# Kernel tuning notes

Hardware: AMD Instinct MI355X
Metric: run time of the kernel (lower is better)

Reference implementation:

```python
import jax, jax.numpy as jnp
import numpy as np

B, N, H, L, E, OUT = 32, 128, 128, 3, 65536, 128
AV, BV = 128, 16  # atom / bond feature vocab sizes
NEG = -1e9


def setup_inputs() -> dict:
    key = jax.random.key(0)
    ks = jax.random.split(key, 20)
    x = jax.random.randint(ks[0], (B * N, 9), 0, AV)          # OGB atom features
    edge_attr = jax.random.randint(ks[1], (E, 3), 0, BV)      # OGB bond features
    # within-graph random edges (PyG requires edges not to cross graphs)
    g = jax.random.randint(ks[2], (E,), 0, B)
    src = jax.random.randint(ks[3], (E,), 0, N)
    dst = jax.random.randint(ks[4], (E,), 0, N)
    edge_index = jnp.stack([g * N + src, g * N + dst])        # [2, E] global node ids
    batch_idx = jnp.repeat(jnp.arange(B), N)                  # equal-size graphs
    s = 0.05
    w = lambda k, *shape: jax.random.normal(k, shape, dtype=jnp.float32) * s
    return {
        "x": x, "edge_attr": edge_attr, "edge_index": edge_index, "batch_idx": batch_idx,
        "atom_emb": w(ks[5], 9, AV, H), "bond_emb": w(ks[6], 3, BV, H),
        "Wm1": w(ks[7], L, 2 * H, H), "bm1": jnp.zeros((L, H), jnp.float32),
        "Wm2": w(ks[8], L, 2 * H, H), "bm2": jnp.zeros((L, H), jnp.float32),
        "We": w(ks[9], L, H, H), "be": jnp.zeros((L, H), jnp.float32),
        "Wg": w(ks[10], L, H, H), "bg": jnp.zeros((L, H), jnp.float32),
        "Wp1": w(ks[11], L, H, H), "bp1": jnp.zeros((L, H), jnp.float32),
        "Wp2": w(ks[12], L, H, H), "bp2": jnp.zeros((L, H), jnp.float32),
        "Wo1": w(ks[13], L, 2 * H, H), "bo1": jnp.zeros((L, H), jnp.float32),
        "Wo2": w(ks[14], L, H, H), "bo2": jnp.zeros((L, H), jnp.float32),
        "ln_s": jnp.ones((L, H), jnp.float32), "ln_b": jnp.zeros((L, H), jnp.float32),
        "Wh1": w(ks[15], H, H), "bh1": jnp.zeros((H,), jnp.float32),
        "Wh2": w(ks[16], H, OUT), "bh2": jnp.zeros((OUT,), jnp.float32),
    }


def reference(x, edge_attr, edge_index, batch_idx, atom_emb, bond_emb,
              Wm1, bm1, Wm2, bm2, We, be, Wg, bg, Wp1, bp1, Wp2, bp2,
              Wo1, bo1, Wo2, bo2, ln_s, ln_b, Wh1, bh1, Wh2, bh2):
    # AtomEncoder / BondEncoder: sum of per-column embeddings
    node_fts = jnp.sum(atom_emb[jnp.arange(9), x], axis=1)        # [B*N, H]
    edge_fts = jnp.sum(bond_emb[jnp.arange(3), edge_attr], axis=1)  # [E, H]
    # to_dense_batch with equal-size graphs == reshape; mask all-True
    node_fts = node_fts.reshape(B, N, H)
    # to_dense_adj: scatter-add edge list into dense [B, N, N] (+features)
    g = edge_index[0] // N
    s_loc = edge_index[0] % N
    d_loc = edge_index[1] % N
    adj = jnp.zeros((B, N, N), jnp.float32).at[g, s_loc, d_loc].add(1.0)
    edge_dense = jnp.zeros((B, N, N, H), jnp.float32).at[g, s_loc, d_loc].add(edge_fts)
    graph_fts = jnp.zeros((B, H), jnp.float32)
    hidden = jnp.zeros_like(node_fts)
    adj_mask = (adj > 0)[..., None]                               # [B, Ns, Nr, 1]
    for l in range(L):  # CLRS-style MPNN layers
        z = jnp.concatenate([node_fts, hidden], axis=-1)          # [B, N, 2H]
        m1 = z @ Wm1[l] + bm1[l]
        m2 = z @ Wm2[l] + bm2[l]
        me = edge_dense @ We[l] + be[l]
        mg = graph_fts @ Wg[l] + bg[l]
        msgs = m1[:, :, None, :] + m2[:, None, :, :] + me + mg[:, None, None, :]
        msgs = jax.nn.relu(msgs)
        msgs = jax.nn.relu(msgs @ Wp1[l] + bp1[l]) @ Wp2[l] + bp2[l]  # msgs MLP [H,H]
        msgs = jnp.max(jnp.where(adj_mask, msgs, NEG), axis=1)   # masked max over senders
        h = jax.nn.relu(z @ Wo1[l] + bo1[l] + msgs @ Wo2[l] + bo2[l])
        mu = h.mean(-1, keepdims=True)
        var = ((h - mu) ** 2).mean(-1, keepdims=True)
        hidden = (h - mu) / jnp.sqrt(var + 1e-5) * ln_s[l] + ln_b[l]
    # masked mean pool (mask is all-True here) + prediction MLP
    graph_emb = hidden.mean(axis=1)                               # [B, H]
    return jax.nn.relu(graph_emb @ Wh1 + bh1) @ Wh2 + bh2         # [B, OUT]
```

## Files before the change

kernel.cpp:

```cpp
#include <hip/hip_runtime.h>
#include <hip/hip_bf16.h>

#define NB_ 32
#define LL_ 3
#define EE_ 65536
#define NODES_ 4096
#define SLOTS_ 524288
#define NEGV -1e9f

typedef _Float16 f16x8 __attribute__((ext_vector_type(8)));
typedef float f32x4 __attribute__((ext_vector_type(4)));

__device__ __forceinline__ unsigned fkey(float f) {
  unsigned b = __float_as_uint(f);
  unsigned m = ((int)b >> 31) | 0x80000000u;
  return b ^ m;
}
__device__ __forceinline__ float funkey(unsigned k) {
  unsigned xm = (k & 0x80000000u) ? 0x80000000u : 0xFFFFFFFFu;
  return __uint_as_float(k ^ xm);
}

__global__ __launch_bounds__(256) void k_pro(const int* __restrict__ x,
    const float* __restrict__ atom_emb, _Float16* __restrict__ zh,
    const float* __restrict__ Wp1, const float* __restrict__ Wp2,
    const float* __restrict__ Wm1, const float* __restrict__ Wm2,
    const float* __restrict__ Wo1, const float* __restrict__ Wo2,
    _Float16* __restrict__ Whf,
    const float* __restrict__ bond_emb, const float* __restrict__ We,
    _Float16* __restrict__ bembWeh,
    const int* __restrict__ ei, int* __restrict__ cnt, int* __restrict__ erank) {
  int blk = blockIdx.x, tid = threadIdx.x;
  if (blk < 2048) {
    int v = blk * 2 + (tid >> 7), t = tid & 127;
    float acc = 0.f;
#pragma unroll
    for (int c = 0; c < 9; c++) {
      int xv = x[v * 9 + c];
      acc += atom_emb[(c * 128 + xv) * 128 + t];
    }
    zh[v * 256 + t] = (_Float16)acc;
    zh[v * 256 + 128 + t] = (_Float16)0.f;
  } else if (blk < 2264) {
    int gid = (blk - 2048) * 256 + tid;
    int lane = gid & 63;
    int llo = lane & 15, lhi = lane >> 4;
    const float* W; int col, kbase;
    if (gid < 12288) {
      int mat = gid >> 11, pos = gid & 2047;
      int fr = pos >> 6; int ct = fr >> 2, kt = fr & 3;
      int lyr = mat >> 1, which = mat & 1;
      W = (which ? Wp2 : Wp1) + lyr * 16384;
      col = ct * 16 + llo; kbase = kt * 32 + lhi * 8;
    } else if (gid < 36864) {
      int q = gid - 12288;
      int lyr = q >> 13, r = q & 8191;
      int fr = r >> 6; int ct = fr >> 3, kt = fr & 7;
      col = ct * 16 + llo; kbase = kt * 32 + lhi * 8;
      if (col < 128) { W = Wm1 + lyr * 32768; }
      else { W = Wm2 + lyr * 32768; col -= 128; }
    } else {
      int q = gid - 36864;
      int lyr = q / 6144, r = q % 6144;
      int fr = r >> 6; int ct = fr / 12, kt = fr % 12;
      col = ct * 16 + llo; kbase = kt * 32 + lhi * 8;
      if (kbase < 256) { W = Wo1 + lyr * 32768; }
      else { W = Wo2 + lyr * 16384; kbase -= 256; }
    }
    f16x8 h;
#pragma unroll
    for (int e = 0; e < 8; e++) h[e] = (_Float16)W[(kbase + e) * 128 + col];
    ((f16x8*)Whf)[gid] = h;
  } else if (blk < 2336) {
    __shared__ float row[2][128];
    int rid = (blk - 2264) * 2 + (tid >> 7);
    int half = tid >> 7, c = tid & 127;
    int l = rid / 48, rr = rid % 48;
    row[half][c] = bond_emb[rr * 128 + c];
    __syncthreads();
    const float* W = We + l * 16384;
    float acc = 0.f;
    for (int k = 0; k < 128; k += 4) {
      acc += row[half][k] * W[k * 128 + c] +
             row[half][k + 1] * W[(k + 1) * 128 + c] +
             row[half][k + 2] * W[(k + 2) * 128 + c] +
             row[half][k + 3] * W[(k + 3) * 128 + c];
    }
    bembWeh[(l * 48 + rr) * 128 + c] = (_Float16)acc;
  } else {
    int e = (blk - 2336) * 256 + tid;
    int s = ei[e], d = ei[EE_ + e];
    int g = s >> 7, i = s & 127, j = d & 127;
    int slot = ((g << 7) + j) * 128 + i;
    erank[e] = atomicAdd(&cnt[slot], 1);
  }
}

__global__ __launch_bounds__(256) void k_scanA(const int* __restrict__ cnt,
    int* __restrict__ basep, int* __restrict__ pairbase,
    int* __restrict__ bsumA, int* __restrict__ bsumF) {
  __shared__ int sA[256], sF[256];
  int t = threadIdx.x, gid = blockIdx.x * 256 + t;
  int v = cnt[gid];
  int f = v > 0 ? 1 : 0;
  sA[t] = v; sF[t] = f; __syncthreads();
  for (int st = 1; st < 256; st <<= 1) {
    int aA = sA[t], aF = sF[t];
    int bA = (t >= st) ? sA[t - st] : 0;
    int bF = (t >= st) ? sF[t - st] : 0;
    __syncthreads();
    sA[t] = aA + bA; sF[t] = aF + bF;
    __syncthreads();
  }
  basep[gid] = sA[t] - v;
  pairbase[gid] = sF[t] - f;
  if (t == 255) { bsumA[blockIdx.x] = sA[255]; bsumF[blockIdx.x] = sF[255]; }
}

__global__ __launch_bounds__(256) void k_scan2d(int* __restrict__ bsumA,
                                                int* __restrict__ bsumF) {
  int* bsum = blockIdx.x ? bsumF : bsumA;
  __shared__ int s[256];
  int t = threadIdx.x;
  int v[8]; int tot = 0;
#pragma unroll
  for (int q = 0; q < 8; q++) { v[q] = bsum[t * 8 + q]; tot += v[q]; }
  s[t] = tot; __syncthreads();
  for (int st = 1; st < 256; st <<= 1) {
    int a = s[t]; int b = (t >= st) ? s[t - st] : 0;
    __syncthreads(); s[t] = a + b; __syncthreads();
  }
  int run = s[t] - tot;
#pragma unroll
  for (int q = 0; q < 8; q++) { int tmp = v[q]; bsum[t * 8 + q] = run; run += tmp; }
}

__global__ __launch_bounds__(256) void k_scanBS(const int* __restrict__ cnt,
    const int* __restrict__ basep, const int* __restrict__ pairbase,
    const int* __restrict__ bsumA, const int* __restrict__ bsumF,
    int* __restrict__ pair_total, int* __restrict__ pair_slot,
    int* __restrict__ pair_off, int* __restrict__ pair_cnt,
    const int* __restrict__ ei, const int* __restrict__ erank,
    int* __restrict__ sorted_e) {
  int blk = blockIdx.x, tid = threadIdx.x;
  if (blk < 2048) {
    int gid = blk * 256 + tid;
    int b = basep[gid] + bsumA[gid >> 8];
    int pb = pairbase[gid] + bsumF[gid >> 8];
    int c = cnt[gid];
    if (c > 0) {
      pair_slot[pb] = gid;
      pair_off[pb] = b;
      pair_cnt[pb] = c;
    }
    if (gid == SLOTS_ - 1) pair_total[0] = pb + (c > 0 ? 1 : 0);
  } else {
    int e = (blk - 2048) * 256 + tid;
    int s = ei[e], d = ei[EE_ + e];
    int g = s >> 7, i = s & 127, j = d & 127;
    int slot = ((g << 7) + j) * 128 + i;
    int pos = basep[slot] + bsumA[slot >> 8] + erank[e];
    sorted_e[pos] = e;
  }
}

__global__ __launch_bounds__(256, 4) void k_m12(const _Float16* __restrict__ zh,
    const _Float16* __restrict__ Whf, const float* __restrict__ bm1,
    const float* __restrict__ bm2, _Float16* __restrict__ mm,
    unsigned* __restrict__ msgs_u, int l) {
  int tid = threadIdx.x;
  {
    int g0 = blockIdx.x * 256 + tid;
    unsigned kneg = fkey(NEGV);
    msgs_u[g0] = kneg;
    msgs_u[g0 + 262144] = kneg;
  }
  int wv = tid >> 6, l64 = tid & 63;
  int llo = l64 & 15, lhi = l64 >> 4;
  int tile = blockIdx.x >> 2;
  int ct = (blockIdx.x & 3) * 4 + wv;
  int row = tile * 16 + llo;
  f16x8 a[8];
#pragma unroll
  for (int kt = 0; kt < 8; kt++)
    a[kt] = *(const f16x8*)(zh + row * 256 + kt * 32 + lhi * 8);
  const f16x8* Bf = (const f16x8*)Whf + 12288 + l * 8192;
  int col = ct * 16 + llo;
  float bv = (col < 128) ? bm1[l * 128 + col] : bm2[l * 128 + col - 128];
  f32x4 acc = {bv, bv, bv, bv};
#pragma unroll
  for (int kt = 0; kt < 8; kt++)
    acc = __builtin_amdgcn_mfma_f32_16x16x32_f16(a[kt], Bf[(ct * 8 + kt) * 64 + l64], acc, 0, 0, 0);
#pragma unroll
  for (int reg = 0; reg < 4; reg++)
    mm[(tile * 16 + lhi * 4 + reg) * 256 + col] = (_Float16)acc[reg];
}

__global__ __launch_bounds__(256, 4) void k_pairs(
    const _Float16* __restrict__ mm,
    const int* __restrict__ pair_slot, const int* __restrict__ pair_off,
    const int* __restrict__ pair_cnt, const int* __restrict__ pair_total,
    const int* __restrict__ sorted_e, const int* __restrict__ edge_attr,
    const _Float16* __restrict__ bembWeh,
    const float* __restrict__ be, const float* __restrict__ bg,
    const _Float16* __restrict__ Whf,
    const float* __restrict__ bp1, const float* __restrict__ bp2,
    unsigned* __restrict__ msgs_u, int l) {
  __shared__ int s_slot[64], s_off[64], s_cnt[64], s_lrow[64];
  __shared__ int s_scan[64];
  __shared__ int s_rid[16];
  __shared__ int s_nrecv;
  __shared__ unsigned Lmax[16 * 128];
  __shared__ _Float16 Uh[64 * 128];
  int P = pair_total[0];
  int pid0 = blockIdx.x * 64;
  if (pid0 >= P) return;
  int tid = threadIdx.x;
  {
    unsigned kneg = fkey(NEGV);
#pragma unroll
    for (int q = 0; q < 8; q++) Lmax[tid + q * 256] = kneg;
  }
  if (tid < 64) {
    int pid = pid0 + tid;
    bool va = pid < P;
    s_slot[tid] = va ? pair_slot[pid] : -1;
    s_off[tid] = va ? pair_off[pid] : 0;
    s_cnt[tid] = va ? pair_cnt[pid] : 0;
  }
  __syncthreads();
  if (tid < 64) {
    int slot = s_slot[tid];
    int r = slot >= 0 ? (slot >> 7) : -1;
    int pr = (tid == 0) ? -2 : (s_slot[tid - 1] >= 0 ? (s_slot[tid - 1] >> 7) : -1);
    s_scan[tid] = (slot >= 0 && r != pr) ? 1 : 0;
  }
  __syncthreads();
  for (int st = 1; st < 64; st <<= 1) {
    int a = 0, b = 0;
    if (tid < 64) { a = s_scan[tid]; b = (tid >= st) ? s_scan[tid - st] : 0; }
    __syncthreads();
    if (tid < 64) s_scan[tid] = a + b;
    __syncthreads();
  }
  if (tid < 64) {
    int slot = s_slot[tid];
    int lr = s_scan[tid] - 1;
    s_lrow[tid] = lr;
    int r = slot >= 0 ? (slot >> 7) : -1;
    int pr = (tid == 0) ? -2 : (s_slot[tid - 1] >= 0 ? (s_slot[tid - 1] >> 7) : -1);
    if (slot >= 0 && r != pr && lr < 16) s_rid[lr] = r;
    if (tid == 63) s_nrecv = s_scan[63];
  }
  __syncthreads();

  int l64 = tid & 63, wv = tid >> 6;
  int llo = l64 & 15, lhi = l64 >> 4;
  int p = wv * 16 + llo;
  int slot = s_slot[p];
  f16x8 a[4];
  if (slot >= 0) {
    int rr = slot >> 7, i = slot & 127, g = slot >> 14;
    int sn = (g << 7) + i;
    float t32[4][8];
#pragma unroll
    for (int kt = 0; kt < 4; kt++) {
      int c0 = kt * 32 + lhi * 8;
      f16x8 v1 = *(const f16x8*)(mm + sn * 256 + c0);
      f16x8 v2 = *(const f16x8*)(mm + rr * 256 + 128 + c0);
      float4 e0 = *(const float4*)(be + l * 128 + c0);
      float4 e1 = *(const float4*)(be + l * 128 + c0 + 4);
      float4 g0 = *(const float4*)(bg + l * 128 + c0);
      float4 g1 = *(const float4*)(bg + l * 128 + c0 + 4);
      t32[kt][0] = (float)v1[0] + (float)v2[0] + e0.x + g0.x;
      t32[kt][1] = (float)v1[1] + (float)v2[1] + e0.y + g0.y;
      t32[kt][2] = (float)v1[2] + (float)v2[2] + e0.z + g0.z;
      t32[kt][3] = (float)v1[3] + (float)v2[3] + e0.w + g0.w;
      t32[kt][4] = (float)v1[4] + (float)v2[4] + e1.x + g1.x;
      t32[kt][5] = (float)v1[5] + (float)v2[5] + e1.y + g1.y;
      t32[kt][6] = (float)v1[6] + (float)v2[6] + e1.z + g1.z;
      t32[kt][7] = (float)v1[7] + (float)v2[7] + e1.w + g1.w;
    }
    int off = s_off[p], cn = s_cnt[p];
    for (int d = 0; d < cn; d++) {
      int eid = sorted_e[off + d];
      int a0 = edge_attr[eid * 3], a1 = edge_attr[eid * 3 + 1],
          a2 = edge_attr[eid * 3 + 2];
      const _Float16* r0 = bembWeh + (l * 48 + a0) * 128;
      const _Float16* r1 = bembWeh + (l * 48 + 16 + a1) * 128;
      const _Float16* r2 = bembWeh + (l * 48 + 32 + a2) * 128;
#pragma unroll
      for (int kt = 0; kt < 4; kt++) {
        int c0 = kt * 32 + lhi * 8;
        f16x8 x0 = *(const f16x8*)(r0 + c0);
        f16x8 x1 = *(const f16x8*)(r1 + c0);
        f16x8 x2 = *(const f16x8*)(r2 + c0);
#pragma unroll
        for (int e = 0; e < 8; e++)
          t32[kt][e] += (float)x0[e] + (float)x1[e] + (float)x2[e];
      }
    }
#pragma unroll
    for (int kt = 0; kt < 4; kt++)
#pragma unroll
      for (int e = 0; e < 8; e++) a[kt][e] = (_Float16)fmaxf(t32[kt][e], 0.f);
  } else {
#pragma unroll
    for (int kt = 0; kt < 4; kt++)
#pragma unroll
      for (int e = 0; e < 8; e++) a[kt][e] = (_Float16)0.f;
  }

  const f16x8* W1f = (const f16x8*)Whf + (l * 2) * 2048;
  const f16x8* W2f = (const f16x8*)Whf + (l * 2 + 1) * 2048;
#pragma unroll
  for (int ct = 0; ct < 8; ct++) {
    int col = ct * 16 + llo;
    float b1 = bp1[l * 128 + col];
    f32x4 acc = {b1, b1, b1, b1};
#pragma unroll
    for (int kt = 0; kt < 4; kt++)
      acc = __builtin_amdgcn_mfma_f32_16x16x32_f16(a[kt], W1f[(ct * 4 + kt) * 64 + l64], acc, 0, 0, 0);
#pragma unroll
    for (int reg = 0; reg < 4; reg++) {
      int wrow = wv * 16 + lhi * 4 + reg;
      int sg = (2 * ct + (llo >> 3)) ^ (wrow & 15);
      Uh[wrow * 128 + sg * 8 + (llo & 7)] = (_Float16)fmaxf(acc[reg], 0.f);
    }
  }
  __syncthreads();
  f16x8 a2[4];
  int arow = wv * 16 + llo;
#pragma unroll
  for (int kt = 0; kt < 4; kt++) {
    int sg = (kt * 4 + lhi) ^ (arow & 15);
    a2[kt] = *(const f16x8*)(Uh + arow * 128 + sg * 8);
  }
#pragma unroll
  for (int ct = 0; ct < 8; ct++) {
    int col = ct * 16 + llo;
    float b2 = bp2[l * 128 + col];
    f32x4 acc = {b2, b2, b2, b2};
#pragma unroll
    for (int kt = 0; kt < 4; kt++)
      acc = __builtin_amdgcn_mfma_f32_16x16x32_f16(a2[kt], W2f[(ct * 4 + kt) * 64 + l64], acc, 0, 0, 0);
    int prev_lr = -2, prev_rr = -1; float run = 0.f;
#pragma unroll
    for (int reg = 0; reg < 4; reg++) {
      int prow = wv * 16 + lhi * 4 + reg;
      int slot2 = s_slot[prow];
      if (slot2 < 0) continue;
      int lr = s_lrow[prow];
      float v = acc[reg];
      if (lr == prev_lr) {
        run = fmaxf(run, v);
      } else {
        if (prev_lr >= 0) {
          if (prev_lr < 16) atomicMax(&Lmax[prev_lr * 128 + col], fkey(run));
          else atomicMax(&msgs_u[prev_rr * 128 + col], fkey(run));
        }
        prev_lr = lr; prev_rr = slot2 >> 7; run = v;
      }
    }
    if (prev_lr >= 0) {
      if (prev_lr < 16) atomicMax(&Lmax[prev_lr * 128 + col], fkey(run));
      else atomicMax(&msgs_u[prev_rr * 128 + col], fkey(run));
    }
  }
  __syncthreads();
  int nr = s_nrecv; if (nr > 16) nr = 16;
  for (int base = 0; base < nr; base += 2) {
    int lr = base + (tid >> 7);
    int col = tid & 127;
    if (lr < nr)
      atomicMax(&msgs_u[s_rid[lr] * 128 + col], Lmax[lr * 128 + col]);
  }
}

__global__ __launch_bounds__(512, 2) void k_olnm12(_Float16* __restrict__ zh,
    unsigned* __restrict__ msgs_u, const _Float16* __restrict__ Whf,
    const float* __restrict__ bo1, const float* __restrict__ bo2,
    const float* __restrict__ ln_s, const float* __restrict__ ln_b,
    const float* __restrict__ bm1, const float* __restrict__ bm2,
    _Float16* __restrict__ mm, int l) {
  __shared__ float sumA[8][16];
  __shared__ float muS[16], rsS[16];
  __shared__ _Float16 hidT[16][132];
  int tid = threadIdx.x;
  int wv = tid >> 6, l64 = tid & 63;
  int llo = l64 & 15, lhi = l64 >> 4;
  int row = blockIdx.x * 16 + llo;
  f16x8 a[12];
#pragma unroll
  for (int kt = 0; kt < 8; kt++)
    a[kt] = *(const f16x8*)(zh + row * 256 + kt * 32 + lhi * 8);
#pragma unroll
  for (int kt = 8; kt < 12; kt++) {
    int k0 = (kt - 8) * 32 + lhi * 8;
    f16x8 h;
#pragma unroll
    for (int e = 0; e < 8; e++) {
      float v = funkey(msgs_u[row * 128 + k0 + e]);
      v = fmaxf(fminf(v, 60000.f), -60000.f);
      h[e] = (_Float16)v;
    }
    a[kt] = h;
  }
  const f16x8* Bo = (const f16x8*)Whf + 36864 + l * 6144;
  int ct = wv, col = ct * 16 + llo;
  float bv = bo1[l * 128 + col] + bo2[l * 128 + col];
  f32x4 acc = {bv, bv, bv, bv};
#pragma unroll
  for (int kt = 0; kt < 12; kt++)
    acc = __builtin_amdgcn_mfma_f32_16x16x32_f16(a[kt], Bo[(ct * 12 + kt) * 64 + l64], acc, 0, 0, 0);
  float h[4];
#pragma unroll
  for (int reg = 0; reg < 4; reg++) h[reg] = fmaxf(acc[reg], 0.f);
#pragma unroll
  for (int reg = 0; reg < 4; reg++) {
    float s = h[reg];
    s += __shfl_xor(s, 1, 64); s += __shfl_xor(s, 2, 64);
    s += __shfl_xor(s, 4, 64); s += __shfl_xor(s, 8, 64);
    if (llo == 0) sumA[wv][lhi * 4 + reg] = s;
  }
  __syncthreads();
  if (tid < 16) {
    float s = 0.f;
#pragma unroll
    for (int w = 0; w < 8; w++) s += sumA[w][tid];
    muS[tid] = s * (1.f / 128.f);
  }
  __syncthreads();
#pragma unroll
  for (int reg = 0; reg < 4; reg++) {
    float d = h[reg] - muS[lhi * 4 + reg];
    float s = d * d;
    s += __shfl_xor(s, 1, 64); s += __shfl_xor(s, 2, 64);
    s += __shfl_xor(s, 4, 64); s += __shfl_xor(s, 8, 64);
    if (llo == 0) sumA[wv][lhi * 4 + reg] = s;
  }
  __syncthreads();
  if (tid < 16) {
    float s = 0.f;
#pragma unroll
    for (int w = 0; w < 8; w++) s += sumA[w][tid];
    rsS[tid] = rsqrtf(s * (1.f / 128.f) + 1e-5f);
  }
  __syncthreads();
  float sc = ln_s[l * 128 + col], bb = ln_b[l * 128 + col];
#pragma unroll
  for (int reg = 0; reg < 4; reg++) {
    int rr = lhi * 4 + reg;
    int wrow = blockIdx.x * 16 + rr;
    _Float16 hh = (_Float16)((h[reg] - muS[rr]) * rsS[rr] * sc + bb);
    zh[wrow * 256 + 128 + col] = hh;
    hidT[rr][col] = hh;
  }
  {
    unsigned kneg = fkey(NEGV);
    int base = blockIdx.x * 2048 + tid;
    msgs_u[base] = kneg;
    msgs_u[base + 512] = kneg;
    msgs_u[base + 1024] = kneg;
    msgs_u[base + 1536] = kneg;
  }
  __syncthreads();
  f16x8 b[4];
#pragma unroll
  for (int kt = 0; kt < 4; kt++)
    b[kt] = *(const f16x8*)(&hidT[llo][kt * 32 + lhi * 8]);
  const f16x8* Bm = (const f16x8*)Whf + 12288 + (l + 1) * 8192;
#pragma unroll
  for (int q = 0; q < 2; q++) {
    int ct2 = wv + q * 8;
    int col2 = ct2 * 16 + llo;
    float bv2 = (col2 < 128) ? bm1[(l + 1) * 128 + col2]
                             : bm2[(l + 1) * 128 + col2 - 128];
    f32x4 acc2 = {bv2, bv2, bv2, bv2};
#pragma unroll
    for (int kt = 0; kt < 4; kt++)
      acc2 = __builtin_amdgcn_mfma_f32_16x16x32_f16(a[kt], Bm[(ct2 * 8 + kt) * 64 + l64], acc2, 0, 0, 0);
#pragma unroll
    for (int kt = 0; kt < 4; kt++)
      acc2 = __builtin_amdgcn_mfma_f32_16x16x32_f16(b[kt], Bm[(ct2 * 8 + 4 + kt) * 64 + l64], acc2, 0, 0, 0);
#pragma unroll
    for (int reg = 0; reg < 4; reg++)
      mm[(blockIdx.x * 16 + lhi * 4 + reg) * 256 + col2] = (_Float16)acc2[reg];
  }
}

__global__ __launch_bounds__(512, 2) void k_out_ln(_Float16* __restrict__ zh,
    const unsigned* __restrict__ msgs_u, const _Float16* __restrict__ Whf,
    const float* __restrict__ bo1, const float* __restrict__ bo2,
    const float* __restrict__ ln_s, const float* __restrict__ ln_b, int l) {
  __shared__ float sumA[8][16];
  __shared__ float muS[16], rsS[16];
  int tid = threadIdx.x;
  int wv = tid >> 6, l64 = tid & 63;
  int llo = l64 & 15, lhi = l64 >> 4;
  int row = blockIdx.x * 16 + llo;
  f16x8 a[12];
#pragma unroll
  for (int kt = 0; kt < 8; kt++)
    a[kt] = *(const f16x8*)(zh + row * 256 + kt * 32 + lhi * 8);
#pragma unroll
  for (int kt = 8; kt < 12; kt++) {
    int k0 = (kt - 8) * 32 + lhi * 8;
    f16x8 h;
#pragma unroll
    for (int e = 0; e < 8; e++) {
      float v = funkey(msgs_u[row * 128 + k0 + e]);
      v = fmaxf(fminf(v, 60000.f), -60000.f);
      h[e] = (_Float16)v;
    }
    a[kt] = h;
  }
  const f16x8* Bf = (const f16x8*)Whf + 36864 + l * 6144;
  int ct = wv, col = ct * 16 + llo;
  float bv = bo1[l * 128 + col] + bo2[l * 128 + col];
  f32x4 acc = {bv, bv, bv, bv};
#pragma unroll
  for (int kt = 0; kt < 12; kt++)
    acc = __builtin_amdgcn_mfma_f32_16x16x32_f16(a[kt], Bf[(ct * 12 + kt) * 64 + l64], acc, 0, 0, 0);
  float h[4];
#pragma unroll
  for (int reg = 0; reg < 4; reg++) h[reg] = fmaxf(acc[reg], 0.f);
#pragma unroll
  for (int reg = 0; reg < 4; reg++) {
    float s = h[reg];
    s += __shfl_xor(s, 1, 64); s += __shfl_xor(s, 2, 64);
    s += __shfl_xor(s, 4, 64); s += __shfl_xor(s, 8, 64);
    if (llo == 0) sumA[wv][lhi * 4 + reg] = s;
  }
  __syncthreads();
  if (tid < 16) {
    float s = 0.f;
#pragma unroll
    for (int w = 0; w < 8; w++) s += sumA[w][tid];
    muS[tid] = s * (1.f / 128.f);
  }
  __syncthreads();
#pragma unroll
  for (int reg = 0; reg < 4; reg++) {
    float d = h[reg] - muS[lhi * 4 + reg];
    float s = d * d;
    s += __shfl_xor(s, 1, 64); s += __shfl_xor(s, 2, 64);
    s += __shfl_xor(s, 4, 64); s += __shfl_xor(s, 8, 64);
    if (llo == 0) sumA[wv][lhi * 4 + reg] = s;
  }
  __syncthreads();
  if (tid < 16) {
    float s = 0.f;
#pragma unroll
    for (int w = 0; w < 8; w++) s += sumA[w][tid];
    rsS[tid] = rsqrtf(s * (1.f / 128.f) + 1e-5f);
  }
  __syncthreads();
  float sc = ln_s[l * 128 + col], bb = ln_b[l * 128 + col];
#pragma unroll
  for (int reg = 0; reg < 4; reg++) {
    int rr = lhi * 4 + reg;
    int wrow = blockIdx.x * 16 + rr;
    zh[wrow * 256 + 128 + col] =
        (_Float16)((h[reg] - muS[rr]) * rsS[rr] * sc + bb);
  }
}

__global__ __launch_bounds__(128) void k_head(const _Float16* __restrict__ zh,
    const float* __restrict__ Wh1, const float* __restrict__ bh1,
    const float* __restrict__ Wh2, const float* __restrict__ bh2,
    float* __restrict__ out) {
  __shared__ float ge[128], p1[128];
  int b = blockIdx.x, t = threadIdx.x;
  float s = 0.f;
  for (int n = 0; n < 128; n++) s += (float)zh[(b * 128 + n) * 256 + 128 + t];
  ge[t] = s * (1.f / 128.f);
  __syncthreads();
  float a = bh1[t];
  for (int k = 0; k < 128; k++) a += ge[k] * Wh1[k * 128 + t];
  p1[t] = fmaxf(a, 0.f);
  __syncthreads();
  float o = bh2[t];
  for (int k = 0; k < 128; k++) o += p1[k] * Wh2[k * 128 + t];
  out[b * 128 + t] = o;
}

extern "C" void kernel_launch(void* const* d_in, const int* in_sizes, int n_in,
                              void* d_out, int out_size, void* d_ws, size_t ws_size,
                              hipStream_t stream) {
  const int* x          = (const int*)d_in[0];
  const int* edge_attr  = (const int*)d_in[1];
  const int* edge_index = (const int*)d_in[2];
  const float* atom_emb = (const float*)d_in[4];
  const float* bond_emb = (const float*)d_in[5];
  const float* Wm1 = (const float*)d_in[6];
  const float* bm1 = (const float*)d_in[7];
  const float* Wm2 = (const float*)d_in[8];
  const float* bm2 = (const float*)d_in[9];
  const float* We  = (const float*)d_in[10];
  const float* be  = (const float*)d_in[11];
  const float* bg  = (const float*)d_in[13];
  const float* Wp1 = (const float*)d_in[14];
  const float* bp1 = (const float*)d_in[15];
  const float* Wp2 = (const float*)d_in[16];
  const float* bp2 = (const float*)d_in[17];
  const float* Wo1 = (const float*)d_in[18];
  const float* bo1 = (const float*)d_in[19];
  const float* Wo2 = (const float*)d_in[20];
  const float* bo2 = (const float*)d_in[21];
  const float* ln_s = (const float*)d_in[22];
  const float* ln_b = (const float*)d_in[23];
  const float* Wh1 = (const float*)d_in[24];
  const float* bh1 = (const float*)d_in[25];
  const float* Wh2 = (const float*)d_in[26];
  const float* bh2 = (const float*)d_in[27];
  float* out = (float*)d_out;

  int* cnt       = (int*)d_ws;
  int* basep     = cnt + SLOTS_;
  int* pairbase  = basep + SLOTS_;
  int* bsumA     = pairbase + SLOTS_;
  int* bsumF     = bsumA + 2048;
  int* pair_tot  = bsumF + 2048;
  int* erank     = pair_tot + 16;
  int* sorted_e  = erank + EE_;
  int* pair_slot = sorted_e + EE_;
  int* pair_off  = pair_slot + EE_;
  int* pair_cnt  = pair_off + EE_;
  unsigned* msgs_u = (unsigned*)(pair_cnt + EE_);
  _Float16* zh   = (_Float16*)(msgs_u + SLOTS_);
  _Float16* mm   = zh + NODES_ * 256;
  _Float16* bembWeh = mm + NODES_ * 256;
  _Float16* Whf  = bembWeh + 3 * 48 * 128;

  hipMemsetAsync(cnt, 0, SLOTS_ * sizeof(int), stream);

  k_pro<<<2592, 256, 0, stream>>>(x, atom_emb, zh, Wp1, Wp2, Wm1, Wm2, Wo1, Wo2,
                                  Whf, bond_emb, We, bembWeh, edge_index, cnt,
                                  erank);
  k_scanA<<<SLOTS_ / 256, 256, 0, stream>>>(cnt, basep, pairbase, bsumA, bsumF);
  k_scan2d<<<2, 256, 0, stream>>>(bsumA, bsumF);
  k_scanBS<<<2304, 256, 0, stream>>>(cnt, basep, pairbase, bsumA, bsumF,
                                     pair_tot, pair_slot, pair_off, pair_cnt,
                                     edge_index, erank, sorted_e);

  k_m12<<<1024, 256, 0, stream>>>(zh, Whf, bm1, bm2, mm, msgs_u, 0);
  k_pairs<<<1024, 256, 0, stream>>>(mm, pair_slot, pair_off, pair_cnt,
                                    pair_tot, sorted_e, edge_attr, bembWeh,
                                    be, bg, Whf, bp1, bp2, msgs_u, 0);
  k_olnm12<<<NODES_ / 16, 512, 0, stream>>>(zh, msgs_u, Whf, bo1, bo2, ln_s,
                                            ln_b, bm1, bm2, mm, 0);
  k_pairs<<<1024, 256, 0, stream>>>(mm, pair_slot, pair_off, pair_cnt,
                                    pair_tot, sorted_e, edge_attr, bembWeh,
                                    be, bg, Whf, bp1, bp2, msgs_u, 1);
  k_olnm12<<<NODES_ / 16, 512, 0, stream>>>(zh, msgs_u, Whf, bo1, bo2, ln_s,
                                            ln_b, bm1, bm2, mm, 1);
  k_pairs<<<1024, 256, 0, stream>>>(mm, pair_slot, pair_off, pair_cnt,
                                    pair_tot, sorted_e, edge_attr, bembWeh,
                                    be, bg, Whf, bp1, bp2, msgs_u, 2);
  k_out_ln<<<NODES_ / 16, 512, 0, stream>>>(zh, msgs_u, Whf, bo1, bo2,
                                            ln_s, ln_b, 2);
  k_head<<<NB_, 128, 0, stream>>>(zh, Wh1, bh1, Wh2, bh2, out);
}
```

Before: 257.3 us.

## Fuse scan stages with last-block election and merge first m12 GEMM into scatter

Removes the separate second-level scan kernel: the last block of the first scan (found through an atomic counter) scans the per-block sums itself. The first layer's m1/m2 GEMM and msgs init are merged into the scatter kernel as extra blocks. The pair-grouping prefix scan in k_pairs now uses wavefront shuffles instead of shared-memory steps with barriers. This cuts two kernel launches and several barriers, at the cost of atomics, fences, and a serial tail in the elected block.

Result: slower. 310.3 us (+20.6%).

```diff
diff --git a/kernel.cpp b/kernel.cpp
--- a/kernel.cpp
+++ b/kernel.cpp
@@ -96,11 +96,12 @@
   }
 }
 
-__global__ __launch_bounds__(256) void k_scanA(const int* __restrict__ cnt,
+__global__ __launch_bounds__(256) void k_scanA2(const int* __restrict__ cnt,
     int* __restrict__ basep, int* __restrict__ pairbase,
-    int* __restrict__ bsumA, int* __restrict__ bsumF) {
+    int* __restrict__ bsumA, int* __restrict__ bsumF, int* __restrict__ done) {
   __shared__ int sA[256], sF[256];
-  int t = threadIdx.x, gid = blockIdx.x * 256 + t;
+  __shared__ int elect;
+  int t = threadIdx.x, blk = blockIdx.x, gid = blk * 256 + t;
   int v = cnt[gid];
   int f = v > 0 ? 1 : 0;
   sA[t] = v; sF[t] = f; __syncthreads();
@@ -114,34 +115,51 @@
   }
   basep[gid] = sA[t] - v;
   pairbase[gid] = sF[t] - f;
-  if (t == 255) { bsumA[blockIdx.x] = sA[255]; bsumF[blockIdx.x] = sF[255]; }
-}
-
-__global__ __launch_bounds__(256) void k_scan2d(int* __restrict__ bsumA,
-                                                int* __restrict__ bsumF) {
-  int* bsum = blockIdx.x ? bsumF : bsumA;
-  __shared__ int s[256];
-  int t = threadIdx.x;
-  int v[8]; int tot = 0;
-#pragma unroll
-  for (int q = 0; q < 8; q++) { v[q] = bsum[t * 8 + q]; tot += v[q]; }
-  s[t] = tot; __syncthreads();
+  if (t == 255) {
+    atomicExch(&bsumA[blk], sA[255]);
+    atomicExch(&bsumF[blk], sF[255]);
+  }
+  __syncthreads();
+  if (t == 0) {
+    __threadfence();
+    elect = (atomicAdd(done, 1) == 2047) ? 1 : 0;
+  }
+  __syncthreads();
+  if (!elect) return;
+  __threadfence();
+  int vA[8], vF[8]; int totA = 0, totF = 0;
+#pragma unroll
+  for (int q = 0; q < 8; q++) {
+    vA[q] = atomicAdd(&bsumA[t * 8 + q], 0); totA += vA[q];
+    vF[q] = atomicAdd(&bsumF[t * 8 + q], 0); totF += vF[q];
+  }
+  sA[t] = totA; sF[t] = totF; __syncthreads();
   for (int st = 1; st < 256; st <<= 1) {
-    int a = s[t]; int b = (t >= st) ? s[t - st] : 0;
-    __syncthreads(); s[t] = a + b; __syncthreads();
-  }
-  int run = s[t] - tot;
-#pragma unroll
-  for (int q = 0; q < 8; q++) { int tmp = v[q]; bsum[t * 8 + q] = run; run += tmp; }
-}
-
-__global__ __launch_bounds__(256) void k_scanBS(const int* __restrict__ cnt,
+    int aA = sA[t], aF = sF[t];
+    int bA = (t >= st) ? sA[t - st] : 0;
+    int bF = (t >= st) ? sF[t - st] : 0;
+    __syncthreads();
+    sA[t] = aA + bA; sF[t] = aF + bF;
+    __syncthreads();
+  }
+  int runA = sA[t] - totA, runF = sF[t] - totF;
+#pragma unroll
+  for (int q = 0; q < 8; q++) {
+    int tA = vA[q]; bsumA[t * 8 + q] = runA; runA += tA;
+    int tF = vF[q]; bsumF[t * 8 + q] = runF; runF += tF;
+  }
+}
+
+__global__ __launch_bounds__(256) void k_scanBSm12(const int* __restrict__ cnt,
     const int* __restrict__ basep, const int* __restrict__ pairbase,
     const int* __restrict__ bsumA, const int* __restrict__ bsumF,
     int* __restrict__ pair_total, int* __restrict__ pair_slot,
     int* __restrict__ pair_off, int* __restrict__ pair_cnt,
     const int* __restrict__ ei, const int* __restrict__ erank,
-    int* __restrict__ sorted_e) {
+    int* __restrict__ sorted_e,
+    const _Float16* __restrict__ zh, const _Float16* __restrict__ Whf,
+    const float* __restrict__ bm1, const float* __restrict__ bm2,
+    _Float16* __restrict__ mm, unsigned* __restrict__ msgs_u) {
   int blk = blockIdx.x, tid = threadIdx.x;
   if (blk < 2048) {
     int gid = blk * 256 + tid;
@@ -154,46 +172,41 @@
       pair_cnt[pb] = c;
     }
     if (gid == SLOTS_ - 1) pair_total[0] = pb + (c > 0 ? 1 : 0);
-  } else {
+  } else if (blk < 2304) {
     int e = (blk - 2048) * 256 + tid;
     int s = ei[e], d = ei[EE_ + e];
     int g = s >> 7, i = s & 127, j = d & 127;
     int slot = ((g << 7) + j) * 128 + i;
     int pos = basep[slot] + bsumA[slot >> 8] + erank[e];
     sorted_e[pos] = e;
-  }
-}
-
-__global__ __launch_bounds__(256, 4) void k_m12(const _Float16* __restrict__ zh,
-    const _Float16* __restrict__ Whf, const float* __restrict__ bm1,
-    const float* __restrict__ bm2, _Float16* __restrict__ mm,
-    unsigned* __restrict__ msgs_u, int l) {
-  int tid = threadIdx.x;
-  {
-    int g0 = blockIdx.x * 256 + tid;
-    unsigned kneg = fkey(NEGV);
-    msgs_u[g0] = kneg;
-    msgs_u[g0 + 262144] = kneg;
-  }
-  int wv = tid >> 6, l64 = tid & 63;
-  int llo = l64 & 15, lhi = l64 >> 4;
-  int tile = blockIdx.x >> 2;
-  int ct = (blockIdx.x & 3) * 4 + wv;
-  int row = tile * 16 + llo;
-  f16x8 a[8];
-#pragma unroll
-  for (int kt = 0; kt < 8; kt++)
-    a[kt] = *(const f16x8*)(zh + row * 256 + kt * 32 + lhi * 8);
-  const f16x8* Bf = (const f16x8*)Whf + 12288 + l * 8192;
-  int col = ct * 16 + llo;
-  float bv = (col < 128) ? bm1[l * 128 + col] : bm2[l * 128 + col - 128];
-  f32x4 acc = {bv, bv, bv, bv};
-#pragma unroll
-  for (int kt = 0; kt < 8; kt++)
-    acc = __builtin_amdgcn_mfma_f32_16x16x32_f16(a[kt], Bf[(ct * 8 + kt) * 64 + l64], acc, 0, 0, 0);
-#pragma unroll
-  for (int reg = 0; reg < 4; reg++)
-    mm[(tile * 16 + lhi * 4 + reg) * 256 + col] = (_Float16)acc[reg];
+  } else {
+    int mblk = blk - 2304;
+    {
+      int g0 = mblk * 256 + tid;
+      unsigned kneg = fkey(NEGV);
+      msgs_u[g0] = kneg;
+      msgs_u[g0 + 262144] = kneg;
+    }
+    int wv = tid >> 6, l64 = tid & 63;
+    int llo = l64 & 15, lhi = l64 >> 4;
+    int tile = mblk >> 2;
+    int ct = (mblk & 3) * 4 + wv;
+    int row = tile * 16 + llo;
+    f16x8 a[8];
+#pragma unroll
+    for (int kt = 0; kt < 8; kt++)
+      a[kt] = *(const f16x8*)(zh + row * 256 + kt * 32 + lhi * 8);
+    const f16x8* Bf = (const f16x8*)Whf + 12288;
+    int col = ct * 16 + llo;
+    float bv = (col < 128) ? bm1[col] : bm2[col - 128];
+    f32x4 acc = {bv, bv, bv, bv};
+#pragma unroll
+    for (int kt = 0; kt < 8; kt++)
+      acc = __builtin_amdgcn_mfma_f32_16x16x32_f16(a[kt], Bf[(ct * 8 + kt) * 64 + l64], acc, 0, 0, 0);
+#pragma unroll
+    for (int reg = 0; reg < 4; reg++)
+      mm[(tile * 16 + lhi * 4 + reg) * 256 + col] = (_Float16)acc[reg];
+  }
 }
 
 __global__ __launch_bounds__(256, 4) void k_pairs(
@@ -207,7 +220,6 @@
     const float* __restrict__ bp1, const float* __restrict__ bp2,
     unsigned* __restrict__ msgs_u, int l) {
   __shared__ int s_slot[64], s_off[64], s_cnt[64], s_lrow[64];
-  __shared__ int s_scan[64];
   __shared__ int s_rid[16];
   __shared__ int s_nrecv;
   __shared__ unsigned Lmax[16 * 128];
@@ -224,33 +236,24 @@
   if (tid < 64) {
     int pid = pid0 + tid;
     bool va = pid < P;
-    s_slot[tid] = va ? pair_slot[pid] : -1;
+    int slot = va ? pair_slot[pid] : -1;
+    s_slot[tid] = slot;
     s_off[tid] = va ? pair_off[pid] : 0;
     s_cnt[tid] = va ? pair_cnt[pid] : 0;
-  }
-  __syncthreads();
-  if (tid < 64) {
-    int slot = s_slot[tid];
     int r = slot >= 0 ? (slot >> 7) : -1;
-    int pr = (tid == 0) ? -2 : (s_slot[tid - 1] >= 0 ? (s_slot[tid - 1] >> 7) : -1);
-    s_scan[tid] = (slot >= 0 && r != pr) ? 1 : 0;
-  }
-  __syncthreads();
-  for (int st = 1; st < 64; st <<= 1) {
-    int a = 0, b = 0;
-    if (tid < 64) { a = s_scan[tid]; b = (tid >= st) ? s_scan[tid - st] : 0; }
-    __syncthreads();
-    if (tid < 64) s_scan[tid] = a + b;
-    __syncthreads();
-  }
-  if (tid < 64) {
-    int slot = s_slot[tid];
-    int lr = s_scan[tid] - 1;
+    int ps = __shfl_up(slot, 1, 64);
+    int pr = (tid == 0) ? -2 : (ps >= 0 ? (ps >> 7) : -1);
+    int flag = (slot >= 0 && r != pr) ? 1 : 0;
+    int val = flag;
+#pragma unroll
+    for (int d = 1; d < 64; d <<= 1) {
+      int o = __shfl_up(val, d, 64);
+      if (tid >= d) val += o;
+    }
+    int lr = val - 1;
     s_lrow[tid] = lr;
-    int r = slot >= 0 ? (slot >> 7) : -1;
-    int pr = (tid == 0) ? -2 : (s_slot[tid - 1] >= 0 ? (s_slot[tid - 1] >> 7) : -1);
-    if (slot >= 0 && r != pr && lr < 16) s_rid[lr] = r;
-    if (tid == 63) s_nrecv = s_scan[63];
+    if (flag && lr < 16) s_rid[lr] = r;
+    if (tid == 63) s_nrecv = val;
   }
   __syncthreads();
 
@@ -617,7 +620,8 @@
   float* out = (float*)d_out;
 
   int* cnt       = (int*)d_ws;
-  int* basep     = cnt + SLOTS_;
+  int* done      = cnt + SLOTS_;
+  int* basep     = done + 16;
   int* pairbase  = basep + SLOTS_;
   int* bsumA     = pairbase + SLOTS_;
   int* bsumF     = bsumA + 2048;
@@ -633,18 +637,18 @@
   _Float16* bembWeh = mm + NODES_ * 256;
   _Float16* Whf  = bembWeh + 3 * 48 * 128;
 
-  hipMemsetAsync(cnt, 0, SLOTS_ * sizeof(int), stream);
+  hipMemsetAsync(cnt, 0, (SLOTS_ + 16) * sizeof(int), stream);
 
   k_pro<<<2592, 256, 0, stream>>>(x, atom_emb, zh, Wp1, Wp2, Wm1, Wm2, Wo1, Wo2,
                                   Whf, bond_emb, We, bembWeh, edge_index, cnt,
                                   erank);
-  k_scanA<<<SLOTS_ / 256, 256, 0, stream>>>(cnt, basep, pairbase, bsumA, bsumF);
-  k_scan2d<<<2, 256, 0, stream>>>(bsumA, bsumF);
-  k_scanBS<<<2304, 256, 0, stream>>>(cnt, basep, pairbase, bsumA, bsumF,
-                                     pair_tot, pair_slot, pair_off, pair_cnt,
-                                     edge_index, erank, sorted_e);
-
-  k_m12<<<1024, 256, 0, stream>>>(zh, Whf, bm1, bm2, mm, msgs_u, 0);
+  k_scanA2<<<SLOTS_ / 256, 256, 0, stream>>>(cnt, basep, pairbase, bsumA,
+                                             bsumF, done);
+  k_scanBSm12<<<3328, 256, 0, stream>>>(cnt, basep, pairbase, bsumA, bsumF,
+                                        pair_tot, pair_slot, pair_off,
+                                        pair_cnt, edge_index, erank, sorted_e,
+                                        zh, Whf, bm1, bm2, mm, msgs_u);
+
   k_pairs<<<1024, 256, 0, stream>>>(mm, pair_slot, pair_off, pair_cnt,
                                     pair_tot, sorted_e, edge_attr, bembWeh,
                                     be, bg, Whf, bp1, bp2, msgs_u, 0);
```
